# Kernel tuning notes

Measured on AMD Instinct MI355X. Metric: run time of the kernel, lower is better.

## Reference

```python
import jax, jax.numpy as jnp
import numpy as np

NUM_CLUSTERS = 256


def setup_inputs() -> dict:
    key = jax.random.key(0)
    k1, k2, k3 = jax.random.split(key, 3)
    a, b, k = 8192, 8192, NUM_CLUSTERS
    w_mat = jax.random.uniform(k1, (a, b), dtype=jnp.float32)
    # softmax-like assignment probabilities over clusters
    p_l = jax.nn.softmax(jax.random.normal(k2, (a, k), dtype=jnp.float32), axis=-1)
    p_r = jax.nn.softmax(jax.random.normal(k3, (b, k), dtype=jnp.float32), axis=-1)
    clusters_p = jnp.ones((k,), dtype=jnp.float32) / k  # uniform init as in module
    return {"w_mat": w_mat, "p_l": p_l, "p_r": p_r, "clusters_p": clusters_p}


def reference(w_mat, p_l, p_r, clusters_p):
    # Algebraically equivalent to:
    #   ((w[:,:,None] * (p_l[:,None,:] + p_r[None,:,:] - 2*p_l[:,None,:]*p_r[None,:,:]))
    #      .sum((0,1)) / clusters_p).sum()
    # without materializing the (a,b,k) tensor.
    row_w = jnp.sum(w_mat, axis=1)            # (a,)  sum_b w[a,b]
    col_w = jnp.sum(w_mat, axis=0)            # (b,)  sum_a w[a,b]
    rs = row_w @ p_l                           # (k,)  sum_{a,b} w * p_l
    cs = col_w @ p_r                           # (k,)  sum_{a,b} w * p_r
    # cross[k] = sum_{a,b} p_l[a,k] * w[a,b] * p_r[b,k]
    cross = jnp.einsum("ka,ak->k", p_l.T @ w_mat, p_r)  # (k,)
    return jnp.sum((rs + cs - 2.0 * cross) / clusters_p)
```

## Files before the change

### kernel.cpp

```cpp
#include <hip/hip_runtime.h>
#include <stdint.h>

#define A_DIM 8192
#define B_DIM 8192
#define K_CL  256
#define NSLAB 8
#define SLABW (B_DIM / NSLAB)
#define NKS   (SLABW / 64)

typedef short bf16x8 __attribute__((ext_vector_type(8)));
typedef float f32x4  __attribute__((ext_vector_type(4)));
typedef float f32x16 __attribute__((ext_vector_type(16)));
typedef unsigned short u16;

__device__ __forceinline__ u16 f2bf(float f) {
    unsigned int u = __float_as_uint(f);
    u += 0x7fffu + ((u >> 16) & 1u);
    return (u16)(u >> 16);
}

__global__ __launch_bounds__(256) void k_prep(const float* __restrict__ pr,
                                              u16* __restrict__ Bpack,
                                              float* __restrict__ out) {
    const int kb2 = blockIdx.x;
    const int t = threadIdx.x;
    if (kb2 == 0 && t == 0) out[0] = 0.0f;
    const int lane = t & 63, wv = t >> 6;
    const int l31 = lane & 31, half = lane >> 5;
#pragma unroll
    for (int ci = 0; ci < 2; ci++) {
        const int c2 = wv * 2 + ci;
        float v[8];
#pragma unroll
        for (int j = 0; j < 8; j++)
            v[j] = pr[(size_t)(kb2 * 16 + half * 8 + j) * K_CL + c2 * 32 + l31];
        union { bf16x8 b; unsigned int u[4]; } o;
#pragma unroll
        for (int j = 0; j < 4; j++)
            o.u[j] = (unsigned int)f2bf(v[2 * j]) | ((unsigned int)f2bf(v[2 * j + 1]) << 16);
        *(bf16x8*)(Bpack + ((size_t)(kb2 * 8 + c2) * 64 + lane) * 8) = o.b;
    }
}

__global__ __launch_bounds__(256, 2) void k_main(const float* __restrict__ w,
                                                 const float* __restrict__ pl,
                                                 const u16* __restrict__ Bpack,
                                                 const float* __restrict__ cp,
                                                 float* __restrict__ out) {
    __shared__ u16 Abuf[2][64 * 64];
    __shared__ float rowsum_s[4][64];
    __shared__ float red[4];

    const int bid = blockIdx.x;
    const int slab = bid & 7;
    const int m0 = (bid >> 3) * 64;
    const int tid = threadIdx.x;
    const int lane = tid & 63, wv = tid >> 6;
    const int l31 = lane & 31, half = lane >> 5;
    const int g4 = lane >> 4, c16 = lane & 15;
    const int kb2base = slab * 64;
    const int swz = (l31 & 7) << 4;

    const float* wthr = w + (size_t)(m0 + wv * 16 + g4) * B_DIM + (size_t)slab * SLABW + c16 * 4;

    int wb[4];
#pragma unroll
    for (int j = 0; j < 4; j++) {
        const int row = wv * 16 + j * 4 + g4;
        wb[j] = row * 128 + ((c16 * 8) ^ ((row & 7) << 4));
    }

    float rcp_cp[2];
#pragma unroll
    for (int n2 = 0; n2 < 2; n2++)
        rcp_cp[n2] = 1.0f / cp[wv * 64 + n2 * 32 + l31];

    f32x16 acc[4];
#pragma unroll
    for (int i = 0; i < 4; i++)
#pragma unroll
        for (int r = 0; r < 16; r++) acc[i][r] = 0.f;

    f32x4 Ga[4], Gb[4];
    bf16x8 BX[8], BY[8];

#define SB0 __builtin_amdgcn_sched_barrier(0)
#define WAITV(n) do { asm volatile("s_waitcnt vmcnt(" #n ")" ::: "memory"); SB0; } while (0)
#define LGKM0BAR do { asm volatile("s_waitcnt lgkmcnt(0)" ::: "memory"); \
                      __builtin_amdgcn_s_barrier(); SB0; } while (0)

#define GLOAD(GS, ks) do {                                                               \
        _Pragma("unroll")                                                                \
        for (int j_ = 0; j_ < 4; j_++)                                                   \
            GS[j_] = *(const f32x4*)(wthr + (size_t)(4 * j_) * B_DIM + (size_t)(ks) * 64); \
        SB0;                                                                             \
    } while (0)

#define LOADB(BS, s_) do {                                                               \
        _Pragma("unroll")                                                                \
        for (int kf_ = 0; kf_ < 4; kf_++)                                                \
            _Pragma("unroll")                                                            \
            for (int n2_ = 0; n2_ < 2; n2_++)                                            \
                BS[kf_ * 2 + n2_] = *(const bf16x8*)(Bpack +                             \
                    ((size_t)((kb2base + (s_) * 4 + kf_) * 8 + wv * 2 + n2_)) * 512 + lane * 8); \
        SB0;                                                                             \
    } while (0)

#define PERM2(hi, lo) __builtin_amdgcn_perm(__float_as_uint(hi), __float_as_uint(lo), 0x07060302u)

#define CONV(GS, bufi) do {                                                              \
        char* lb_ = (char*)&Abuf[(bufi)][0];                                             \
        _Pragma("unroll")                                                                \
        for (int j_ = 0; j_ < 4; j_++) {                                                 \
            uint2 p_;                                                                    \
            p_.x = PERM2(GS[j_][1], GS[j_][0]);                                          \
            p_.y = PERM2(GS[j_][3], GS[j_][2]);                                          \
            *(uint2*)(lb_ + wb[j_]) = p_;                                                \
        }                                                                                \
    } while (0)

#define COMP(bufi, BS) do {                                                              \
        const char* ab_ = (const char*)&Abuf[(bufi)][0];                                 \
        _Pragma("unroll")                                                                \
        for (int kf_ = 0; kf_ < 4; kf_++) {                                              \
            const int ko_ = (kf_ * 32 + half * 16) ^ swz;                                \
            bf16x8 a0_ = *(const bf16x8*)(ab_ + l31 * 128 + ko_);                        \
            bf16x8 a1_ = *(const bf16x8*)(ab_ + (32 + l31) * 128 + ko_);                 \
            acc[0] = __builtin_amdgcn_mfma_f32_32x32x16_bf16(a0_, BS[kf_ * 2 + 0], acc[0], 0, 0, 0); \
            acc[1] = __builtin_amdgcn_mfma_f32_32x32x16_bf16(a0_, BS[kf_ * 2 + 1], acc[1], 0, 0, 0); \
            acc[2] = __builtin_amdgcn_mfma_f32_32x32x16_bf16(a1_, BS[kf_ * 2 + 0], acc[2], 0, 0, 0); \
            acc[3] = __builtin_amdgcn_mfma_f32_32x32x16_bf16(a1_, BS[kf_ * 2 + 1], acc[3], 0, 0, 0); \
        }                                                                                \
        SB0;                                                                             \
    } while (0)

#define BODY(s_, GS, BS, WG, WB, DOG, DOB) do {                                          \
        WAITV(WG);                                    \
        CONV(GS, ((s_) + 1) & 1);                                                        \
        WAITV(WB);                            \
        COMP((s_) & 1, BS);                                                              \
        if (DOB) LOADB(BS, (s_) + 2);                        \
        if (DOG) GLOAD(GS, (s_) + 3);                       \
        LGKM0BAR;                                                                        \
    } while (0)

    LOADB(BX, 0);
    GLOAD(Ga, 0);
    GLOAD(Gb, 1);
    WAITV(4);
    CONV(Ga, 0);
    LOADB(BY, 1);
    GLOAD(Ga, 2);
    LGKM0BAR;

    for (int s = 0; s < NKS - 4; s += 2) {
        BODY(s,     Gb, BX, 12, 4, 1, 1);
        BODY(s + 1, Ga, BY, 12, 4, 1, 1);
    }
    BODY(12, Gb, BX, 12, 4, 1, 1);
    BODY(13, Ga, BY, 12, 4, 0, 1);
    BODY(14, Gb, BX,  8, 0, 0, 0);
    COMP(1, BY);

#undef BODY
#undef COMP
#undef CONV
#undef PERM2
#undef LOADB
#undef GLOAD

#pragma unroll
    for (int mf = 0; mf < 2; mf++) {
#pragma unroll
        for (int reg = 0; reg < 16; reg++) {
            float v = acc[mf * 2 + 0][reg] + acc[mf * 2 + 1][reg];
            v += __shfl_xor(v, 1, 64);
            v += __shfl_xor(v, 2, 64);
            v += __shfl_xor(v, 4, 64);
            v += __shfl_xor(v, 8, 64);
            v += __shfl_xor(v, 16, 64);
            const int lrow = mf * 32 + (reg & 3) + 8 * (reg >> 2) + 4 * half;
            if (l31 == 0) rowsum_s[wv][lrow] = v;
        }
    }
    __syncthreads();

    float tot = 0.f;
#pragma unroll
    for (int mf = 0; mf < 2; mf++) {
#pragma unroll
        for (int reg = 0; reg < 16; reg++) {
            const int lrow = mf * 32 + (reg & 3) + 8 * (reg >> 2) + 4 * half;
            const float rs = rowsum_s[0][lrow] + rowsum_s[1][lrow]
                           + rowsum_s[2][lrow] + rowsum_s[3][lrow];
            const float* plrow = pl + (size_t)(m0 + lrow) * K_CL + wv * 64 + l31;
#pragma unroll
            for (int n2 = 0; n2 < 2; n2++) {
                const float q = acc[mf * 2 + n2][reg];
                const float p = plrow[n2 * 32];
                tot += (q + p * (rs - 2.0f * q)) * rcp_cp[n2];
            }
        }
    }
    for (int o = 32; o; o >>= 1) tot += __shfl_down(tot, o, 64);
    if (lane == 0) red[wv] = tot;
    __syncthreads();
    if (tid == 0) atomicAdd(out, red[0] + red[1] + red[2] + red[3]);

#undef WAITV
#undef LGKM0BAR
#undef SB0
}

extern "C" void kernel_launch(void* const* d_in, const int* in_sizes, int n_in,
                              void* d_out, int out_size, void* d_ws, size_t ws_size,
                              hipStream_t stream) {
    const float* w  = (const float*)d_in[0];
    const float* pl = (const float*)d_in[1];
    const float* pr = (const float*)d_in[2];
    const float* cp = (const float*)d_in[3];
    float* out = (float*)d_out;

    u16* Bpack = (u16*)d_ws;

    k_prep<<<dim3(512), dim3(256), 0, stream>>>(pr, Bpack, out);
    k_main<<<dim3(128 * NSLAB), dim3(256), 0, stream>>>(w, pl, Bpack, cp, out);
}
```

Before: 84.68 us.

## Split k_main across 8 waves and compute row sums from fp32 loads

The block grows from 256 to 512 threads, so each of 8 waves owns 32 clusters with two 32x32 accumulators instead of 4 waves with four. Each thread now issues two global loads of w per step instead of four. Row sums of w are accumulated in fp32 directly from the loaded values, replacing the shuffle reduction over the MFMA outputs. The pipeline is reordered so B for the next step loads before the wait, and launch bounds rise to 4 blocks per CU to raise occupancy, which trades fewer registers per thread and more duplicated LDS A-tile reads across waves.

```diff
diff --git a/kernel.cpp b/kernel.cpp
--- a/kernel.cpp
+++ b/kernel.cpp
@@ -42,14 +42,14 @@
     }
 }
 
-__global__ __launch_bounds__(256, 2) void k_main(const float* __restrict__ w,
+__global__ __launch_bounds__(512, 4) void k_main(const float* __restrict__ w,
                                                  const float* __restrict__ pl,
                                                  const u16* __restrict__ Bpack,
                                                  const float* __restrict__ cp,
                                                  float* __restrict__ out) {
     __shared__ u16 Abuf[2][64 * 64];
-    __shared__ float rowsum_s[4][64];
-    __shared__ float red[4];
+    __shared__ float rowsum_s[64];
+    __shared__ float red[8];
 
     const int bid = blockIdx.x;
     const int slab = bid & 7;
@@ -57,155 +57,144 @@
     const int tid = threadIdx.x;
     const int lane = tid & 63, wv = tid >> 6;
     const int l31 = lane & 31, half = lane >> 5;
-    const int g4 = lane >> 4, c16 = lane & 15;
     const int kb2base = slab * 64;
-    const int swz = (l31 & 7) << 4;
-
-    const float* wthr = w + (size_t)(m0 + wv * 16 + g4) * B_DIM + (size_t)slab * SLABW + c16 * 4;
-
-    int wb[4];
-#pragma unroll
-    for (int j = 0; j < 4; j++) {
-        const int row = wv * 16 + j * 4 + g4;
-        wb[j] = row * 128 + ((c16 * 8) ^ ((row & 7) << 4));
-    }
-
-    float rcp_cp[2];
-#pragma unroll
-    for (int n2 = 0; n2 < 2; n2++)
-        rcp_cp[n2] = 1.0f / cp[wv * 64 + n2 * 32 + l31];
-
-    f32x16 acc[4];
-#pragma unroll
-    for (int i = 0; i < 4; i++)
-#pragma unroll
-        for (int r = 0; r < 16; r++) acc[i][r] = 0.f;
-
-    f32x4 Ga[4], Gb[4];
-    bf16x8 BX[8], BY[8];
+
+    const int srow = tid >> 4;
+    const int scol8 = (tid & 15) * 8;
+    const float* wthr = w + (size_t)(m0 + srow) * B_DIM + (size_t)slab * SLABW + (tid & 15) * 4;
+
+    const int wb0 = srow * 128 + (scol8 ^ ((srow & 7) << 4));
+    const int wb1 = wb0 + 32 * 128;
+
+    float sm0 = 0.f, sm1 = 0.f;
+    f32x16 acc0, acc1;
+#pragma unroll
+    for (int r = 0; r < 16; r++) { acc0[r] = 0.f; acc1[r] = 0.f; }
+
+    f32x4 GA0, GA1, GB0, GB1;
+    bf16x8 BX[4], BY[4];
 
 #define SB0 __builtin_amdgcn_sched_barrier(0)
 #define WAITV(n) do { asm volatile("s_waitcnt vmcnt(" #n ")" ::: "memory"); SB0; } while (0)
 #define LGKM0BAR do { asm volatile("s_waitcnt lgkmcnt(0)" ::: "memory"); \
                       __builtin_amdgcn_s_barrier(); SB0; } while (0)
 
-#define GLOAD(GS, ks) do {                                                               \
-        _Pragma("unroll")                                                                \
-        for (int j_ = 0; j_ < 4; j_++)                                                   \
-            GS[j_] = *(const f32x4*)(wthr + (size_t)(4 * j_) * B_DIM + (size_t)(ks) * 64); \
+#define GLOAD(G0_, G1_, ks) do {                                                         \
+        G0_ = *(const f32x4*)(wthr + (size_t)(ks) * 64);                                 \
+        G1_ = *(const f32x4*)(wthr + 32 * B_DIM + (size_t)(ks) * 64);                    \
         SB0;                                                                             \
     } while (0)
 
 #define LOADB(BS, s_) do {                                                               \
         _Pragma("unroll")                                                                \
         for (int kf_ = 0; kf_ < 4; kf_++)                                                \
-            _Pragma("unroll")                                                            \
-            for (int n2_ = 0; n2_ < 2; n2_++)                                            \
-                BS[kf_ * 2 + n2_] = *(const bf16x8*)(Bpack +                             \
-                    ((size_t)((kb2base + (s_) * 4 + kf_) * 8 + wv * 2 + n2_)) * 512 + lane * 8); \
+            BS[kf_] = *(const bf16x8*)(Bpack +                                           \
+                ((size_t)((kb2base + (s_) * 4 + kf_) * 8 + wv)) * 512 + lane * 8);       \
         SB0;                                                                             \
     } while (0)
 
 #define PERM2(hi, lo) __builtin_amdgcn_perm(__float_as_uint(hi), __float_as_uint(lo), 0x07060302u)
 
-#define CONV(GS, bufi) do {                                                              \
+#define CONV(G0_, G1_, bufi) do {                                                        \
+        sm0 += G0_[0] + G0_[1] + G0_[2] + G0_[3];                                        \
+        sm1 += G1_[0] + G1_[1] + G1_[2] + G1_[3];                                        \
+        uint2 p0_, p1_;                                                                  \
+        p0_.x = PERM2(G0_[1], G0_[0]); p0_.y = PERM2(G0_[3], G0_[2]);                    \
+        p1_.x = PERM2(G1_[1], G1_[0]); p1_.y = PERM2(G1_[3], G1_[2]);                    \
         char* lb_ = (char*)&Abuf[(bufi)][0];                                             \
-        _Pragma("unroll")                                                                \
-        for (int j_ = 0; j_ < 4; j_++) {                                                 \
-            uint2 p_;                                                                    \
-            p_.x = PERM2(GS[j_][1], GS[j_][0]);                                          \
-            p_.y = PERM2(GS[j_][3], GS[j_][2]);                                          \
-            *(uint2*)(lb_ + wb[j_]) = p_;                                                \
-        }                                                                                \
-    } while (0)
-
-#define COMP(bufi, BS) do {                                                              \
+        *(uint2*)(lb_ + wb0) = p0_;                                                      \
+        *(uint2*)(lb_ + wb1) = p1_;                                                      \
+    } while (0)
+
+#define COMPUTE(bufi, BS) do {                                                           \
         const char* ab_ = (const char*)&Abuf[(bufi)][0];                                 \
+        const int swz_ = (l31 & 7) << 4;                                                 \
         _Pragma("unroll")                                                                \
         for (int kf_ = 0; kf_ < 4; kf_++) {                                              \
-            const int ko_ = (kf_ * 32 + half * 16) ^ swz;                                \
+            const int ko_ = (kf_ * 32 + half * 16) ^ swz_;                               \
             bf16x8 a0_ = *(const bf16x8*)(ab_ + l31 * 128 + ko_);                        \
             bf16x8 a1_ = *(const bf16x8*)(ab_ + (32 + l31) * 128 + ko_);                 \
-            acc[0] = __builtin_amdgcn_mfma_f32_32x32x16_bf16(a0_, BS[kf_ * 2 + 0], acc[0], 0, 0, 0); \
-            acc[1] = __builtin_amdgcn_mfma_f32_32x32x16_bf16(a0_, BS[kf_ * 2 + 1], acc[1], 0, 0, 0); \
-            acc[2] = __builtin_amdgcn_mfma_f32_32x32x16_bf16(a1_, BS[kf_ * 2 + 0], acc[2], 0, 0, 0); \
-            acc[3] = __builtin_amdgcn_mfma_f32_32x32x16_bf16(a1_, BS[kf_ * 2 + 1], acc[3], 0, 0, 0); \
+            acc0 = __builtin_amdgcn_mfma_f32_32x32x16_bf16(a0_, BS[kf_], acc0, 0, 0, 0); \
+            acc1 = __builtin_amdgcn_mfma_f32_32x32x16_bf16(a1_, BS[kf_], acc1, 0, 0, 0); \
         }                                                                                \
         SB0;                                                                             \
     } while (0)
 
-#define BODY(s_, GS, BS, WG, WB, DOG, DOB) do {                                          \
-        WAITV(WG);                                    \
-        CONV(GS, ((s_) + 1) & 1);                                                        \
-        WAITV(WB);                            \
-        COMP((s_) & 1, BS);                                                              \
-        if (DOB) LOADB(BS, (s_) + 2);                        \
-        if (DOG) GLOAD(GS, (s_) + 3);                       \
+#define BODY(s_, BC, BN, GS0, GS1, WN, DOB, DOG, DOCONV) do {                            \
+        if (DOB) LOADB(BN, (s_) + 1);                                                    \
+        WAITV(WN);                                           \
+        if (DOCONV) CONV(GS0, GS1, ((s_) + 1) & 1);                                      \
+        if (DOG) GLOAD(GS0, GS1, (s_) + 3);                                              \
+        COMPUTE((s_) & 1, BC);                                                           \
         LGKM0BAR;                                                                        \
     } while (0)
 
+    GLOAD(GA0, GA1, 0);
     LOADB(BX, 0);
-    GLOAD(Ga, 0);
-    GLOAD(Gb, 1);
-    WAITV(4);
-    CONV(Ga, 0);
-    LOADB(BY, 1);
-    GLOAD(Ga, 2);
+    GLOAD(GB0, GB1, 1);
+    WAITV(6);
+    CONV(GA0, GA1, 0);
+    GLOAD(GA0, GA1, 2);
     LGKM0BAR;
 
-    for (int s = 0; s < NKS - 4; s += 2) {
-        BODY(s,     Gb, BX, 12, 4, 1, 1);
-        BODY(s + 1, Ga, BY, 12, 4, 1, 1);
-    }
-    BODY(12, Gb, BX, 12, 4, 1, 1);
-    BODY(13, Ga, BY, 12, 4, 0, 1);
-    BODY(14, Gb, BX,  8, 0, 0, 0);
-    COMP(1, BY);
+    for (int s = 0; s < 12; s += 2) {
+        BODY(s,     BX, BY, GB0, GB1, 6, 1, 1, 1);
+        BODY(s + 1, BY, BX, GA0, GA1, 6, 1, 1, 1);
+    }
+    BODY(12, BX, BY, GB0, GB1, 6, 1, 1, 1);
+    BODY(13, BY, BX, GA0, GA1, 6, 1, 0, 1);
+    BODY(14, BX, BY, GB0, GB1, 4, 1, 0, 1);
+    WAITV(0);
+    COMPUTE(1, BY);
 
 #undef BODY
-#undef COMP
+#undef COMPUTE
 #undef CONV
 #undef PERM2
 #undef LOADB
 #undef GLOAD
 
-#pragma unroll
-    for (int mf = 0; mf < 2; mf++) {
-#pragma unroll
-        for (int reg = 0; reg < 16; reg++) {
-            float v = acc[mf * 2 + 0][reg] + acc[mf * 2 + 1][reg];
-            v += __shfl_xor(v, 1, 64);
-            v += __shfl_xor(v, 2, 64);
-            v += __shfl_xor(v, 4, 64);
-            v += __shfl_xor(v, 8, 64);
-            v += __shfl_xor(v, 16, 64);
-            const int lrow = mf * 32 + (reg & 3) + 8 * (reg >> 2) + 4 * half;
-            if (l31 == 0) rowsum_s[wv][lrow] = v;
+    {
+        float v0 = sm0, v1 = sm1;
+#pragma unroll
+        for (int o = 1; o <= 8; o <<= 1) {
+            v0 += __shfl_xor(v0, o, 64);
+            v1 += __shfl_xor(v1, o, 64);
+        }
+        if ((lane & 15) == 0) {
+            rowsum_s[srow] = v0;
+            rowsum_s[32 + srow] = v1;
         }
     }
     __syncthreads();
 
+    const float rcp = 1.0f / cp[wv * 32 + l31];
     float tot = 0.f;
 #pragma unroll
-    for (int mf = 0; mf < 2; mf++) {
-#pragma unroll
-        for (int reg = 0; reg < 16; reg++) {
-            const int lrow = mf * 32 + (reg & 3) + 8 * (reg >> 2) + 4 * half;
-            const float rs = rowsum_s[0][lrow] + rowsum_s[1][lrow]
-                           + rowsum_s[2][lrow] + rowsum_s[3][lrow];
-            const float* plrow = pl + (size_t)(m0 + lrow) * K_CL + wv * 64 + l31;
-#pragma unroll
-            for (int n2 = 0; n2 < 2; n2++) {
-                const float q = acc[mf * 2 + n2][reg];
-                const float p = plrow[n2 * 32];
-                tot += (q + p * (rs - 2.0f * q)) * rcp_cp[n2];
-            }
+    for (int reg = 0; reg < 16; reg++) {
+        const int r0 = (reg & 3) + 8 * (reg >> 2) + 4 * half;
+        {
+            const float rs = rowsum_s[r0];
+            const float p = pl[(size_t)(m0 + r0) * K_CL + wv * 32 + l31];
+            const float q = acc0[reg];
+            tot += (q + p * (rs - 2.0f * q)) * rcp;
+        }
+        {
+            const float rs = rowsum_s[32 + r0];
+            const float p = pl[(size_t)(m0 + 32 + r0) * K_CL + wv * 32 + l31];
+            const float q = acc1[reg];
+            tot += (q + p * (rs - 2.0f * q)) * rcp;
         }
     }
     for (int o = 32; o; o >>= 1) tot += __shfl_down(tot, o, 64);
     if (lane == 0) red[wv] = tot;
     __syncthreads();
-    if (tid == 0) atomicAdd(out, red[0] + red[1] + red[2] + red[3]);
+    if (tid == 0) {
+        float s = 0.f;
+#pragma unroll
+        for (int i = 0; i < 8; i++) s += red[i];
+        atomicAdd(out, s);
+    }
 
 #undef WAITV
 #undef LGKM0BAR
@@ -224,5 +213,5 @@
     u16* Bpack = (u16*)d_ws;
 
     k_prep<<<dim3(512), dim3(256), 0, stream>>>(pr, Bpack, out);
-    k_main<<<dim3(128 * NSLAB), dim3(256), 0, stream>>>(w, pl, Bpack, cp, out);
-}
+    k_main<<<dim3(128 * NSLAB), dim3(512), 0, stream>>>(w, pl, Bpack, cp, out);
+}
```

New measurement: 140.8 us. 1.66x slower.

## Restructure main kernel to full-row 32-row tiles with 8 waves and fused rowsums

Applied to the files above, without the earlier changes.

Each block now owns 32 full rows of w instead of a 64-row by 1024-column slab. The 8 waves each cover 32 clusters, and the loop runs over the whole B dimension with a finer-grained prefetch pipeline of B fragments. Row sums are taken directly from the fp32 loads in the convert step rather than reduced out of the MFMA accumulators. This removes the per-slab split and cuts the 8x partial atomics per row group, but each B fragment is now reused by only one 32-row MFMA tile, so traffic on the packed p_r operand rises and there are fewer blocks (256).

```diff
diff --git a/kernel.cpp b/kernel.cpp
--- a/kernel.cpp
+++ b/kernel.cpp
@@ -4,9 +4,7 @@
 #define A_DIM 8192
 #define B_DIM 8192
 #define K_CL  256
-#define NSLAB 8
-#define SLABW (B_DIM / NSLAB)
-#define NKS   (SLABW / 64)
+#define NSTEP 32
 
 typedef short bf16x8 __attribute__((ext_vector_type(8)));
 typedef float f32x4  __attribute__((ext_vector_type(4)));
@@ -42,67 +40,55 @@
     }
 }
 
-__global__ __launch_bounds__(256, 2) void k_main(const float* __restrict__ w,
+__global__ __launch_bounds__(512, 2) void k_main(const float* __restrict__ w,
                                                  const float* __restrict__ pl,
                                                  const u16* __restrict__ Bpack,
                                                  const float* __restrict__ cp,
                                                  float* __restrict__ out) {
-    __shared__ u16 Abuf[2][64 * 64];
-    __shared__ float rowsum_s[4][64];
-    __shared__ float red[4];
+    __shared__ u16 Abuf[2][32 * 256];
+    __shared__ float rowsum_s[32];
+    __shared__ float red[8];
 
     const int bid = blockIdx.x;
-    const int slab = bid & 7;
-    const int m0 = (bid >> 3) * 64;
+    const int m0 = bid * 32;
     const int tid = threadIdx.x;
     const int lane = tid & 63, wv = tid >> 6;
     const int l31 = lane & 31, half = lane >> 5;
-    const int g4 = lane >> 4, c16 = lane & 15;
-    const int kb2base = slab * 64;
-    const int swz = (l31 & 7) << 4;
-
-    const float* wthr = w + (size_t)(m0 + wv * 16 + g4) * B_DIM + (size_t)slab * SLABW + c16 * 4;
+
+    const float* wthr = w + (size_t)(m0 + wv * 4) * B_DIM + lane * 4;
 
     int wb[4];
 #pragma unroll
     for (int j = 0; j < 4; j++) {
-        const int row = wv * 16 + j * 4 + g4;
-        wb[j] = row * 128 + ((c16 * 8) ^ ((row & 7) << 4));
-    }
-
-    float rcp_cp[2];
-#pragma unroll
-    for (int n2 = 0; n2 < 2; n2++)
-        rcp_cp[n2] = 1.0f / cp[wv * 64 + n2 * 32 + l31];
-
-    f32x16 acc[4];
-#pragma unroll
-    for (int i = 0; i < 4; i++)
-#pragma unroll
-        for (int r = 0; r < 16; r++) acc[i][r] = 0.f;
-
-    f32x4 Ga[4], Gb[4];
-    bf16x8 BX[8], BY[8];
+        const int row = wv * 4 + j;
+        wb[j] = row * 512 + ((lane * 8) ^ ((row & 31) << 4));
+    }
+
+    f32x16 acc;
+#pragma unroll
+    for (int r = 0; r < 16; r++) acc[r] = 0.f;
+    float sm[4] = {0.f, 0.f, 0.f, 0.f};
+
+    f32x4 GA[4], GB[4];
+    bf16x8 Q0[4], Q1[4], Q2[4], Q3[4];
 
 #define SB0 __builtin_amdgcn_sched_barrier(0)
 #define WAITV(n) do { asm volatile("s_waitcnt vmcnt(" #n ")" ::: "memory"); SB0; } while (0)
 #define LGKM0BAR do { asm volatile("s_waitcnt lgkmcnt(0)" ::: "memory"); \
                       __builtin_amdgcn_s_barrier(); SB0; } while (0)
 
-#define GLOAD(GS, ks) do {                                                               \
+#define GLOADA(GS, s_) do {                                                              \
         _Pragma("unroll")                                                                \
         for (int j_ = 0; j_ < 4; j_++)                                                   \
-            GS[j_] = *(const f32x4*)(wthr + (size_t)(4 * j_) * B_DIM + (size_t)(ks) * 64); \
+            GS[j_] = *(const f32x4*)(wthr + (size_t)j_ * B_DIM + (size_t)(s_) * 256);    \
         SB0;                                                                             \
     } while (0)
 
-#define LOADB(BS, s_) do {                                                               \
-        _Pragma("unroll")                                                                \
-        for (int kf_ = 0; kf_ < 4; kf_++)                                                \
-            _Pragma("unroll")                                                            \
-            for (int n2_ = 0; n2_ < 2; n2_++)                                            \
-                BS[kf_ * 2 + n2_] = *(const bf16x8*)(Bpack +                             \
-                    ((size_t)((kb2base + (s_) * 4 + kf_) * 8 + wv * 2 + n2_)) * 512 + lane * 8); \
+#define LOADQ(Qs, s_, q_) do {                                                           \
+        _Pragma("unroll")                                                                \
+        for (int i_ = 0; i_ < 4; i_++)                                                   \
+            Qs[i_] = *(const bf16x8*)(Bpack +                                            \
+                (size_t)(((s_) * 16 + (q_) * 4 + i_) * 8 + wv) * 512 + lane * 8);        \
         SB0;                                                                             \
     } while (0)
 
@@ -112,6 +98,7 @@
         char* lb_ = (char*)&Abuf[(bufi)][0];                                             \
         _Pragma("unroll")                                                                \
         for (int j_ = 0; j_ < 4; j_++) {                                                 \
+            sm[j_] += GS[j_][0] + GS[j_][1] + GS[j_][2] + GS[j_][3];                     \
             uint2 p_;                                                                    \
             p_.x = PERM2(GS[j_][1], GS[j_][0]);                                          \
             p_.y = PERM2(GS[j_][3], GS[j_][2]);                                          \
@@ -119,93 +106,90 @@
         }                                                                                \
     } while (0)
 
-#define COMP(bufi, BS) do {                                                              \
-        const char* ab_ = (const char*)&Abuf[(bufi)][0];                                 \
-        _Pragma("unroll")                                                                \
-        for (int kf_ = 0; kf_ < 4; kf_++) {                                              \
-            const int ko_ = (kf_ * 32 + half * 16) ^ swz;                                \
-            bf16x8 a0_ = *(const bf16x8*)(ab_ + l31 * 128 + ko_);                        \
-            bf16x8 a1_ = *(const bf16x8*)(ab_ + (32 + l31) * 128 + ko_);                 \
-            acc[0] = __builtin_amdgcn_mfma_f32_32x32x16_bf16(a0_, BS[kf_ * 2 + 0], acc[0], 0, 0, 0); \
-            acc[1] = __builtin_amdgcn_mfma_f32_32x32x16_bf16(a0_, BS[kf_ * 2 + 1], acc[1], 0, 0, 0); \
-            acc[2] = __builtin_amdgcn_mfma_f32_32x32x16_bf16(a1_, BS[kf_ * 2 + 0], acc[2], 0, 0, 0); \
-            acc[3] = __builtin_amdgcn_mfma_f32_32x32x16_bf16(a1_, BS[kf_ * 2 + 1], acc[3], 0, 0, 0); \
+#define QUAD(q_, Qs, bufi) do {                                                          \
+        const char* ab_ = (const char*)&Abuf[(bufi)][0] + l31 * 512;                     \
+        _Pragma("unroll")                                                                \
+        for (int i_ = 0; i_ < 4; i_++) {                                                 \
+            const int kf_ = (q_) * 4 + i_;                                               \
+            bf16x8 a_ = *(const bf16x8*)(ab_ + ((kf_ * 32 + half * 16) ^ (l31 << 4)));   \
+            acc = __builtin_amdgcn_mfma_f32_32x32x16_bf16(a_, Qs[i_], acc, 0, 0, 0);     \
         }                                                                                \
         SB0;                                                                             \
     } while (0)
 
-#define BODY(s_, GS, BS, WG, WB, DOG, DOB) do {                                          \
-        WAITV(WG);                                    \
-        CONV(GS, ((s_) + 1) & 1);                                                        \
-        WAITV(WB);                            \
-        COMP((s_) & 1, BS);                                                              \
-        if (DOB) LOADB(BS, (s_) + 2);                        \
-        if (DOG) GLOAD(GS, (s_) + 3);                       \
+#define BODY(s_, GC, GN, DOA, DOB0, W2, W5, W9, W12) do {                                \
+        LOADQ(Q1, s_, 1); LOADQ(Q2, s_, 2);                                              \
+        WAITV(W2);                            \
+        QUAD(0, Q0, (s_) & 1);                                                           \
+        LOADQ(Q3, s_, 3);                                                                \
+        WAITV(W5);                                         \
+        CONV(GC, ((s_) + 1) & 1);                                                        \
+        QUAD(1, Q1, (s_) & 1);                                                           \
+        if (DOB0) LOADQ(Q0, (s_) + 1, 0);                                                \
+        WAITV(W9);                                                        \
+        QUAD(2, Q2, (s_) & 1);                                                           \
+        if (DOA) GLOADA(GN, (s_) + 2);                                                   \
+        WAITV(W12);                       \
+        QUAD(3, Q3, (s_) & 1);                                                           \
         LGKM0BAR;                                                                        \
     } while (0)
 
-    LOADB(BX, 0);
-    GLOAD(Ga, 0);
-    GLOAD(Gb, 1);
-    WAITV(4);
-    CONV(Ga, 0);
-    LOADB(BY, 1);
-    GLOAD(Ga, 2);
+    GLOADA(GA, 0);
+    LOADQ(Q0, 0, 0);
+    GLOADA(GB, 1);
+    WAITV(8);
+    CONV(GA, 0);
     LGKM0BAR;
 
-    for (int s = 0; s < NKS - 4; s += 2) {
-        BODY(s,     Gb, BX, 12, 4, 1, 1);
-        BODY(s + 1, Ga, BY, 12, 4, 1, 1);
-    }
-    BODY(12, Gb, BX, 12, 4, 1, 1);
-    BODY(13, Ga, BY, 12, 4, 0, 1);
-    BODY(14, Gb, BX,  8, 0, 0, 0);
-    COMP(1, BY);
+    for (int s = 0; s < 30; s += 2) {
+        BODY(s,     GB, GA, 1, 1, 12, 8, 8, 8);
+        BODY(s + 1, GA, GB, 1, 1, 12, 8, 8, 8);
+    }
+    BODY(30, GB, GA, 0, 1, 12, 8, 8, 4);
+    {
+        LOADQ(Q1, 31, 1); LOADQ(Q2, 31, 2);
+        WAITV(8);  QUAD(0, Q0, 1);
+        LOADQ(Q3, 31, 3);
+        WAITV(8);  QUAD(1, Q1, 1);
+        WAITV(4);  QUAD(2, Q2, 1);
+        WAITV(0);  QUAD(3, Q3, 1);
+    }
 
 #undef BODY
-#undef COMP
+#undef QUAD
 #undef CONV
 #undef PERM2
-#undef LOADB
-#undef GLOAD
-
-#pragma unroll
-    for (int mf = 0; mf < 2; mf++) {
-#pragma unroll
-        for (int reg = 0; reg < 16; reg++) {
-            float v = acc[mf * 2 + 0][reg] + acc[mf * 2 + 1][reg];
-            v += __shfl_xor(v, 1, 64);
-            v += __shfl_xor(v, 2, 64);
-            v += __shfl_xor(v, 4, 64);
-            v += __shfl_xor(v, 8, 64);
-            v += __shfl_xor(v, 16, 64);
-            const int lrow = mf * 32 + (reg & 3) + 8 * (reg >> 2) + 4 * half;
-            if (l31 == 0) rowsum_s[wv][lrow] = v;
-        }
+#undef LOADQ
+#undef GLOADA
+
+#pragma unroll
+    for (int j = 0; j < 4; j++) {
+        float v = sm[j];
+#pragma unroll
+        for (int o = 1; o <= 32; o <<= 1) v += __shfl_xor(v, o, 64);
+        if (lane == 0) rowsum_s[wv * 4 + j] = v;
     }
     __syncthreads();
 
+    const float rcp = 1.0f / cp[wv * 32 + l31];
     float tot = 0.f;
 #pragma unroll
-    for (int mf = 0; mf < 2; mf++) {
-#pragma unroll
-        for (int reg = 0; reg < 16; reg++) {
-            const int lrow = mf * 32 + (reg & 3) + 8 * (reg >> 2) + 4 * half;
-            const float rs = rowsum_s[0][lrow] + rowsum_s[1][lrow]
-                           + rowsum_s[2][lrow] + rowsum_s[3][lrow];
-            const float* plrow = pl + (size_t)(m0 + lrow) * K_CL + wv * 64 + l31;
-#pragma unroll
-            for (int n2 = 0; n2 < 2; n2++) {
-                const float q = acc[mf * 2 + n2][reg];
-                const float p = plrow[n2 * 32];
-                tot += (q + p * (rs - 2.0f * q)) * rcp_cp[n2];
-            }
-        }
+    for (int reg = 0; reg < 16; reg++) {
+        const int lrow = (reg & 3) + 8 * (reg >> 2) + 4 * half;
+        const float rs = rowsum_s[lrow];
+        const float p = pl[(size_t)(m0 + lrow) * K_CL + wv * 32 + l31];
+        const float q = acc[reg];
+        tot += (q + p * (rs - 2.0f * q)) * rcp;
     }
     for (int o = 32; o; o >>= 1) tot += __shfl_down(tot, o, 64);
     if (lane == 0) red[wv] = tot;
     __syncthreads();
-    if (tid == 0) atomicAdd(out, red[0] + red[1] + red[2] + red[3]);
+    if (tid == 0) {
+        float s = 0.f;
+#pragma unroll
+        for (int i = 0; i < 8; i++) s += red[i];
+        atomicAdd(out, s);
+    }
 
 #undef WAITV
 #undef LGKM0BAR
@@ -224,5 +208,5 @@
     u16* Bpack = (u16*)d_ws;
 
     k_prep<<<dim3(512), dim3(256), 0, stream>>>(pr, Bpack, out);
-    k_main<<<dim3(128 * NSLAB), dim3(256), 0, stream>>>(w, pl, Bpack, cp, out);
-}
+    k_main<<<dim3(A_DIM / 32), dim3(512), 0, stream>>>(w, pl, Bpack, cp, out);
+}
```

Result: faster. 76.73 us (-9.4%).
